# Optimization experiments

Hardware: AMD Instinct MI355X
Metric: run time of the kernel (lower is better)

The kernel has to match this reference:

```python
import jax, jax.numpy as jnp
import numpy as np

N, D_IN, D_QK, D_V = 8192, 1024, 128, 128

def setup_inputs() -> dict:
    key = jax.random.key(0)
    k1, k2, k3, k4 = jax.random.split(key, 4)
    return {
        "x": jax.random.normal(k1, (N, D_IN), dtype=jnp.float32),
        "W_q": jax.random.normal(k2, (D_IN, D_QK), dtype=jnp.float32),
        "W_k": jax.random.normal(k3, (D_IN, D_QK), dtype=jnp.float32),
        "W_v": jax.random.normal(k4, (D_IN, D_V), dtype=jnp.float32),
    }

def reference(x, W_q, W_k, W_v):
    Q = x @ W_q          # [N, d_qk]
    K = x @ W_k          # [N, d_qk]
    V = x @ W_v          # [N, d_v]
    scale = 1.0 / jnp.sqrt(jnp.asarray(W_q.shape[1], dtype=Q.dtype))
    S = jnp.einsum("nd,md->nm", Q, K) * scale  # [N, N]
    A = jax.nn.softmax(S, axis=1)
    return A @ V         # [N, d_v]
```

## Files before the change

kernel.cpp:

```cpp
#include <hip/hip_runtime.h>
#include <cstdint>
#include <cstddef>

#define NTOK 8192
#define DIN  1024
#define DH   128
#define KVB  64

typedef __attribute__((ext_vector_type(4))) float f32x4;
typedef __attribute__((ext_vector_type(16))) float f32x16;
typedef __bf16 bf16x8 __attribute__((ext_vector_type(8)));
typedef unsigned short u16x8 __attribute__((ext_vector_type(8)));
typedef unsigned int u32x4 __attribute__((ext_vector_type(4)));

__device__ __forceinline__ unsigned short f2bf(float f){
  union { float f; unsigned u; } x; x.f = f;
  unsigned r = x.u + 0x7FFFu + ((x.u >> 16) & 1u);
  return (unsigned short)(r >> 16);
}
__device__ __forceinline__ float bf2f(unsigned short b){
  union { unsigned u; float f; } x; x.u = ((unsigned)b) << 16;
  return x.f;
}
__device__ __forceinline__ unsigned cvtpk_bf16(float lo, float hi){
  unsigned r;
  asm volatile("v_cvt_pk_bf16_f32 %0, %1, %2" : "=v"(r) : "v"(lo), "v"(hi));
  return r;
}
__device__ __forceinline__ void gload16(const void* g, void* l){
  using gp_t = const __attribute__((address_space(1))) char*;
  using lp_t = __attribute__((address_space(3))) char*;
  __builtin_amdgcn_global_load_lds((gp_t)(uintptr_t)g, (lp_t)(uint32_t)(uintptr_t)l, 16, 0, 0);
}

__global__ void k_wsplit(const float* __restrict__ Wq, const float* __restrict__ Wk,
                         const float* __restrict__ Wv,
                         unsigned short* __restrict__ WhT, unsigned short* __restrict__ WlT){
  int e = blockIdx.x * 256 + threadIdx.x;
  int n = e >> 10, k = e & 1023;
  const float* W = (n < 128) ? Wq : ((n < 256) ? Wk : Wv);
  float v = W[(size_t)k * 128 + (n & 127)];
  unsigned short h = f2bf(v);
  WhT[e] = h;
  WlT[e] = f2bf(v - bf2f(h));
}

__global__ void k_xsplit(const float* __restrict__ x,
                         unsigned short* __restrict__ xh, unsigned short* __restrict__ xl){
  size_t i = ((size_t)blockIdx.x * 256 + threadIdx.x) * 8;
  f32x4 a = *(const f32x4*)(x + i);
  f32x4 b = *(const f32x4*)(x + i + 4);
  u16x8 h, l;
  #pragma unroll
  for (int j = 0; j < 4; ++j){
    unsigned short h0 = f2bf(a[j]); h[j] = h0;   l[j]   = f2bf(a[j] - bf2f(h0));
    unsigned short h1 = f2bf(b[j]); h[4+j] = h1; l[4+j] = f2bf(b[j] - bf2f(h1));
  }
  *(u16x8*)(xh + i) = h;
  *(u16x8*)(xl + i) = l;
}

__global__ __launch_bounds__(256, 3) void k_proj(
    const unsigned short* __restrict__ xh, const unsigned short* __restrict__ xl,
    const unsigned short* __restrict__ WhT, const unsigned short* __restrict__ WlT,
    unsigned short* __restrict__ Qh, unsigned short* __restrict__ Ql,
    unsigned short* __restrict__ Kh, unsigned short* __restrict__ Kl,
    unsigned short* __restrict__ Vt){
  __shared__ __align__(16) char smem[32768];
  const int lane = threadIdx.x & 63, wid = threadIdx.x >> 6;
  const int l15 = lane & 15, lk = lane >> 4;
  const int bm = blockIdx.x;
  const int by = blockIdx.y;
  const int bt = by >> 1, nh = by & 1;
  const int wm = wid >> 1, wn = wid & 1;

  const int srow = lane >> 3;
  const int gc8  = (lane & 7) ^ srow;
  const unsigned short* gsrc;
  char* ldst;
  int grow0;
  if (wid == 0){      gsrc = xh;  grow0 = bm*64;            ldst = smem; }
  else if (wid == 1){ gsrc = xl;  grow0 = bm*64;            ldst = smem + 8192; }
  else if (wid == 2){ gsrc = WhT; grow0 = bt*128 + nh*64;   ldst = smem + 16384; }
  else {              gsrc = WlT; grow0 = bt*128 + nh*64;   ldst = smem + 24576; }
  const unsigned short* gbase = gsrc + (size_t)(grow0 + srow)*DIN + gc8*8;
  const bool stage_on = (bt < 2) || (wid == 0) || (wid == 2);

  f32x4 acc[2][2] = {};

  for (int t = 0; t < 16; ++t){
    if (stage_on){
      #pragma unroll
      for (int i = 0; i < 8; ++i)
        gload16(gbase + (size_t)i*8*DIN + t*64, ldst + i*1024);
    }
    __syncthreads();

    bf16x8 a_h[2][2], a_l[2][2], b_h[2][2], b_l[2][2];
    const unsigned sw = (unsigned)(l15 & 7);
    #pragma unroll
    for (int mf = 0; mf < 2; ++mf)
      #pragma unroll
      for (int kc = 0; kc < 2; ++kc){
        unsigned rA = (unsigned)(wm*32 + mf*16 + l15);
        unsigned offA = rA*128u + ((((unsigned)(kc*4 + lk)) ^ sw)*16u);
        a_h[mf][kc] = *(const bf16x8*)(const void*)(smem + offA);
        unsigned rB = (unsigned)(wn*32 + mf*16 + l15);
        unsigned offB = rB*128u + ((((unsigned)(kc*4 + lk)) ^ sw)*16u);
        b_h[mf][kc] = *(const bf16x8*)(const void*)(smem + 16384 + offB);
        if (bt < 2){
          a_l[mf][kc] = *(const bf16x8*)(const void*)(smem + 8192 + offA);
          b_l[mf][kc] = *(const bf16x8*)(const void*)(smem + 24576 + offB);
        }
      }
    #pragma unroll
    for (int mf = 0; mf < 2; ++mf)
      #pragma unroll
      for (int nf = 0; nf < 2; ++nf)
        #pragma unroll
        for (int kc = 0; kc < 2; ++kc){
          acc[mf][nf] = __builtin_amdgcn_mfma_f32_16x16x32_bf16(a_h[mf][kc], b_h[nf][kc], acc[mf][nf], 0,0,0);
          if (bt < 2){
            acc[mf][nf] = __builtin_amdgcn_mfma_f32_16x16x32_bf16(a_h[mf][kc], b_l[nf][kc], acc[mf][nf], 0,0,0);
            acc[mf][nf] = __builtin_amdgcn_mfma_f32_16x16x32_bf16(a_l[mf][kc], b_h[nf][kc], acc[mf][nf], 0,0,0);
          }
        }
    __syncthreads();
  }

  const float qscale = 0.08838834764831845f;
  #pragma unroll
  for (int mf = 0; mf < 2; ++mf){
    #pragma unroll
    for (int nf = 0; nf < 2; ++nf){
      #pragma unroll
      for (int r = 0; r < 4; ++r){
        int row = bm*64 + wm*32 + mf*16 + lk*4 + r;
        int col = nh*64 + wn*32 + nf*16 + l15;
        float v = acc[mf][nf][r];
        if (bt == 0){
          v *= qscale;
          unsigned short h = f2bf(v);
          Qh[(size_t)row*DH + col] = h;
          Ql[(size_t)row*DH + col] = f2bf(v - bf2f(h));
        } else if (bt == 1){
          unsigned short h = f2bf(v);
          Kh[(size_t)row*DH + col] = h;
          Kl[(size_t)row*DH + col] = f2bf(v - bf2f(h));
        } else {
          Vt[(size_t)col*NTOK + row] = f2bf(v);
        }
      }
    }
  }
}

__global__ __launch_bounds__(256, 2) void k_flash(
    const unsigned short* __restrict__ Qh, const unsigned short* __restrict__ Ql,
    const unsigned short* __restrict__ Kh, const unsigned short* __restrict__ Kl,
    const unsigned short* __restrict__ Vt,
    float* __restrict__ Opart, float* __restrict__ mpart, float* __restrict__ lpart,
    int ksplit){
  __shared__ __align__(16) char smem[49152];
  char* smemc = smem;
  const int tid = threadIdx.x;
  const int lane = tid & 63, wid = tid >> 6;
  const int l31 = lane & 31, hi = lane >> 5;
  const int qb = blockIdx.x / ksplit, ks = blockIdx.x - qb*ksplit;
  const int q0w = qb*128 + wid*32;
  const int kvlen = NTOK / ksplit;
  const int kvbase = ks * kvlen;
  const int NT = kvlen / KVB;

  bf16x8 qh[8], ql[8];
  #pragma unroll
  for (int kc = 0; kc < 8; ++kc){
    size_t off = (size_t)(q0w + l31)*DH + kc*16 + hi*8;
    qh[kc] = *(const bf16x8*)(const void*)(Qh + off);
    ql[kc] = *(const bf16x8*)(const void*)(Ql + off);
  }

  int gK[4], gV[4], ldsO[4];
  #pragma unroll
  for (int i = 0; i < 4; ++i){
    int g = 4*wid + i;
    int rk = 4*g + (lane >> 4);
    gK[i] = rk*DH + (((lane & 15) ^ (rk & 7))*8);
    int rv = 8*g + (lane >> 3);
    gV[i] = rv*NTOK + (((lane & 7) ^ (lane >> 3))*8);
    ldsO[i] = g*1024;
  }

  #define STAGE(kv0_) do { int _o = (kv0_)*DH;                          \
    _Pragma("unroll")                                                   \
    for (int i = 0; i < 4; ++i){                                        \
      gload16(Kh + (size_t)(_o + gK[i]), smemc + ldsO[i]);              \
      gload16(Kl + (size_t)(_o + gK[i]), smemc + 16384 + ldsO[i]);      \
      gload16(Vt + (size_t)(gV[i] + (kv0_)), smemc + 32768 + ldsO[i]);  \
    } } while(0)

  STAGE(kvbase);
  __syncthreads();

  f32x16 o[4] = {};
  float m_run = -3.0e38f, l_run = 0.f;

  for (int t = 0; t < NT; ++t){
    f32x16 s0 = {}, s1 = {};
    __builtin_amdgcn_s_setprio(1);
    #pragma unroll
    for (int kc = 0; kc < 8; ++kc){
      int r0 = l31;
      unsigned off0 = (unsigned)r0*256u + ((((unsigned)(kc*2 + hi)) ^ (unsigned)(r0 & 7))*16u);
      bf16x8 kh0 = *(const bf16x8*)(const void*)(smemc + off0);
      bf16x8 kl0 = *(const bf16x8*)(const void*)(smemc + 16384 + off0);
      s0 = __builtin_amdgcn_mfma_f32_32x32x16_bf16(kh0, qh[kc], s0, 0,0,0);
      s0 = __builtin_amdgcn_mfma_f32_32x32x16_bf16(kl0, qh[kc], s0, 0,0,0);
      s0 = __builtin_amdgcn_mfma_f32_32x32x16_bf16(kh0, ql[kc], s0, 0,0,0);
      int r1 = 32 + l31;
      unsigned off1 = (unsigned)r1*256u + ((((unsigned)(kc*2 + hi)) ^ (unsigned)(r1 & 7))*16u);
      bf16x8 kh1 = *(const bf16x8*)(const void*)(smemc + off1);
      bf16x8 kl1 = *(const bf16x8*)(const void*)(smemc + 16384 + off1);
      s1 = __builtin_amdgcn_mfma_f32_32x32x16_bf16(kh1, qh[kc], s1, 0,0,0);
      s1 = __builtin_amdgcn_mfma_f32_32x32x16_bf16(kl1, qh[kc], s1, 0,0,0);
      s1 = __builtin_amdgcn_mfma_f32_32x32x16_bf16(kh1, ql[kc], s1, 0,0,0);
    }
    __builtin_amdgcn_s_setprio(0);

    float pmax = s0[0];
    #pragma unroll
    for (int i = 1; i < 16; ++i) pmax = fmaxf(pmax, s0[i]);
    #pragma unroll
    for (int i = 0; i < 16; ++i) pmax = fmaxf(pmax, s1[i]);
    pmax = fmaxf(pmax, __shfl_xor(pmax, 32));
    if (!__all(pmax - m_run <= 8.f)){
      float mnew = fmaxf(m_run, pmax);
      float corr = __expf(m_run - mnew);
      l_run *= corr;
      #pragma unroll
      for (int dblk = 0; dblk < 4; ++dblk)
        #pragma unroll
        for (int i = 0; i < 16; ++i) o[dblk][i] *= corr;
      m_run = mnew;
    }
    float tsum = 0.f;
    #pragma unroll
    for (int i = 0; i < 16; ++i){ s0[i] = __expf(s0[i] - m_run); tsum += s0[i]; }
    #pragma unroll
    for (int i = 0; i < 16; ++i){ s1[i] = __expf(s1[i] - m_run); tsum += s1[i]; }
    tsum += __shfl_xor(tsum, 32);
    l_run += tsum;

    __builtin_amdgcn_s_setprio(1);
    #pragma unroll
    for (int b = 0; b < 4; ++b){
      f32x16 sv = (b & 2) ? s1 : s0;
      const int base = 8*(b & 1);
      unsigned w0 = cvtpk_bf16(sv[base+0], sv[base+1]);
      unsigned w1 = cvtpk_bf16(sv[base+2], sv[base+3]);
      unsigned w2 = cvtpk_bf16(sv[base+4], sv[base+5]);
      unsigned w3 = cvtpk_bf16(sv[base+6], sv[base+7]);
      unsigned sx0 = (unsigned)__shfl_xor((int)w0, 32);
      unsigned sx1 = (unsigned)__shfl_xor((int)w1, 32);
      unsigned sx2 = (unsigned)__shfl_xor((int)w2, 32);
      unsigned sx3 = (unsigned)__shfl_xor((int)w3, 32);
      u32x4 pw;
      pw[0] = hi ? sx2 : w0;
      pw[1] = hi ? sx3 : w1;
      pw[2] = hi ? w2 : sx0;
      pw[3] = hi ? w3 : sx1;
      bf16x8 pB = __builtin_bit_cast(bf16x8, pw);
      #pragma unroll
      for (int dblk = 0; dblk < 4; ++dblk){
        int rv = dblk*32 + l31;
        unsigned offv = 32768u + (unsigned)rv*128u +
                        ((((unsigned)(b*2 + hi)) ^ (unsigned)(rv & 7))*16u);
        bf16x8 vf = *(const bf16x8*)(const void*)(smemc + offv);
        o[dblk] = __builtin_amdgcn_mfma_f32_32x32x16_bf16(vf, pB, o[dblk], 0,0,0);
      }
    }
    __builtin_amdgcn_s_setprio(0);

    __syncthreads();
    if (t + 1 < NT) STAGE(kvbase + (t+1)*KVB);
    __syncthreads();
  }
  #undef STAGE

  float* Op = Opart + ((size_t)ks*NTOK + q0w + l31)*DH;
  #pragma unroll
  for (int dblk = 0; dblk < 4; ++dblk)
    #pragma unroll
    for (int g = 0; g < 4; ++g){
      f32x4 q4 = { o[dblk][4*g+0], o[dblk][4*g+1], o[dblk][4*g+2], o[dblk][4*g+3] };
      *(f32x4*)(Op + dblk*32 + 8*g + 4*hi) = q4;
    }
  if (hi == 0){
    mpart[(size_t)ks*NTOK + q0w + l31] = m_run;
    lpart[(size_t)ks*NTOK + q0w + l31] = l_run;
  }
}

__global__ void k_merge(const float* __restrict__ Opart, const float* __restrict__ mpart,
                        const float* __restrict__ lpart, float* __restrict__ out, int ksplit){
  int gid = blockIdx.x*256 + threadIdx.x;
  int n = gid >> 5, c4 = (gid & 31) * 4;
  float M = -1e30f;
  for (int ks = 0; ks < ksplit; ++ks) M = fmaxf(M, mpart[(size_t)ks*NTOK + n]);
  float L = 0.f;
  f32x4 acc = {0.f, 0.f, 0.f, 0.f};
  for (int ks = 0; ks < ksplit; ++ks){
    float w = __expf(mpart[(size_t)ks*NTOK + n] - M);
    L += lpart[(size_t)ks*NTOK + n] * w;
    f32x4 op = *(const f32x4*)(Opart + ((size_t)ks*NTOK + n)*DH + c4);
    acc += op * w;
  }
  float inv = 1.f / L;
  *(f32x4*)(out + (size_t)n*DH + c4) = acc * inv;
}

extern "C" void kernel_launch(void* const* d_in, const int* in_sizes, int n_in,
                              void* d_out, int out_size, void* d_ws, size_t ws_size,
                              hipStream_t stream){
  const float* x  = (const float*)d_in[0];
  const float* Wq = (const float*)d_in[1];
  const float* Wk = (const float*)d_in[2];
  const float* Wv = (const float*)d_in[3];
  float* out = (float*)d_out;

  char* ws = (char*)d_ws;
  const size_t SZ_WT = (size_t)384*1024*2;
  const size_t SZ_X  = (size_t)NTOK*DIN*2;
  const size_t SZ_QK = (size_t)NTOK*DH*2;
  size_t off = 0;
  unsigned short* WhT = (unsigned short*)(ws + off); off += SZ_WT;
  unsigned short* WlT = (unsigned short*)(ws + off); off += SZ_WT;
  unsigned short* xh  = (unsigned short*)(ws + off); off += SZ_X;
  unsigned short* xl  = (unsigned short*)(ws + off); off += SZ_X;
  unsigned short* Qh  = (unsigned short*)(ws + off); off += SZ_QK;
  unsigned short* Ql  = (unsigned short*)(ws + off); off += SZ_QK;
  unsigned short* Kh  = (unsigned short*)(ws + off); off += SZ_QK;
  unsigned short* Kl  = (unsigned short*)(ws + off); off += SZ_QK;
  unsigned short* Vt  = (unsigned short*)(ws + off); off += SZ_QK;

  int ksplit = 8;
  while (ksplit > 1 &&
         off + (size_t)ksplit*(NTOK*(size_t)DH*4 + 2*NTOK*4) > ws_size)
    ksplit >>= 1;
  float* Opart = (float*)(ws + off); off += (size_t)ksplit*NTOK*DH*4;
  float* mpart = (float*)(ws + off); off += (size_t)ksplit*NTOK*4;
  float* lpart = (float*)(ws + off); off += (size_t)ksplit*NTOK*4;

  k_wsplit<<<dim3((384*1024)/256), dim3(256), 0, stream>>>(Wq, Wk, Wv, WhT, WlT);
  k_xsplit<<<dim3((NTOK*DIN)/(256*8)), dim3(256), 0, stream>>>(x, xh, xl);
  k_proj  <<<dim3(NTOK/64, 6), dim3(256), 0, stream>>>(xh, xl, WhT, WlT, Qh, Ql, Kh, Kl, Vt);
  k_flash <<<dim3((NTOK/128)*ksplit), dim3(256), 0, stream>>>(Qh, Ql, Kh, Kl, Vt,
                                                              Opart, mpart, lpart, ksplit);
  k_merge <<<dim3(NTOK*32/256), dim3(256), 0, stream>>>(Opart, mpart, lpart, out, ksplit);
}
```

Baseline: 184.0 us.

## Double-buffer K/V tiles in LDS and widen flash blocks to 512 threads

The flash kernel now uses 8 waves per block covering 256 query rows, so each K/V tile staged in LDS is shared by twice as many waves. LDS is doubled to hold two buffers, and the next tile's async load is issued before computing on the current one, which removes one barrier per iteration and overlaps global loads with MFMA work. The cost is 96KB of LDS per block and half as many blocks in the grid, which limits occupancy to one block per CU and may leave CUs idle.

```diff
diff --git a/kernel.cpp b/kernel.cpp
--- a/kernel.cpp
+++ b/kernel.cpp
@@ -155,19 +155,19 @@
   }
 }
 
-__global__ __launch_bounds__(256, 2) void k_flash(
+__global__ __launch_bounds__(512, 2) void k_flash(
     const unsigned short* __restrict__ Qh, const unsigned short* __restrict__ Ql,
     const unsigned short* __restrict__ Kh, const unsigned short* __restrict__ Kl,
     const unsigned short* __restrict__ Vt,
     float* __restrict__ Opart, float* __restrict__ mpart, float* __restrict__ lpart,
     int ksplit){
-  __shared__ __align__(16) char smem[49152];
+  __shared__ __align__(16) char smem[98304];
   char* smemc = smem;
   const int tid = threadIdx.x;
   const int lane = tid & 63, wid = tid >> 6;
   const int l31 = lane & 31, hi = lane >> 5;
   const int qb = blockIdx.x / ksplit, ks = blockIdx.x - qb*ksplit;
-  const int q0w = qb*128 + wid*32;
+  const int q0w = qb*256 + wid*32;
   const int kvlen = NTOK / ksplit;
   const int kvbase = ks * kvlen;
   const int NT = kvlen / KVB;
@@ -180,45 +180,50 @@
     ql[kc] = *(const bf16x8*)(const void*)(Ql + off);
   }
 
-  int gK[4], gV[4], ldsO[4];
-  #pragma unroll
-  for (int i = 0; i < 4; ++i){
-    int g = 4*wid + i;
-    int rk = 4*g + (lane >> 4);
-    gK[i] = rk*DH + (((lane & 15) ^ (rk & 7))*8);
-    int rv = 8*g + (lane >> 3);
-    gV[i] = rv*NTOK + (((lane & 7) ^ (lane >> 3))*8);
-    ldsO[i] = g*1024;
-  }
-
-  #define STAGE(kv0_) do { int _o = (kv0_)*DH;                          \
-    _Pragma("unroll")                                                   \
-    for (int i = 0; i < 4; ++i){                                        \
-      gload16(Kh + (size_t)(_o + gK[i]), smemc + ldsO[i]);              \
-      gload16(Kl + (size_t)(_o + gK[i]), smemc + 16384 + ldsO[i]);      \
-      gload16(Vt + (size_t)(gV[i] + (kv0_)), smemc + 32768 + ldsO[i]);  \
+  #define STAGE(kv0_, bufo_) do {                                          \
+    _Pragma("unroll")                                                      \
+    for (int i_ = 0; i_ < 6; ++i_){                                        \
+      int g_ = 6*wid + i_;                                                 \
+      const unsigned short* gp_; unsigned lo_;                             \
+      if (g_ < 16){                                                        \
+        int rk_ = 4*g_ + (lane >> 4);                                      \
+        gp_ = Kh + (size_t)(kv0_)*DH + rk_*DH + (((lane&15)^(rk_&7))*8);   \
+        lo_ = (unsigned)g_*1024u;                                          \
+      } else if (g_ < 32){                                                 \
+        int g2_ = g_ - 16; int rk_ = 4*g2_ + (lane >> 4);                  \
+        gp_ = Kl + (size_t)(kv0_)*DH + rk_*DH + (((lane&15)^(rk_&7))*8);   \
+        lo_ = 16384u + (unsigned)g2_*1024u;                                \
+      } else {                                                             \
+        int g2_ = g_ - 32; int rv_ = 8*g2_ + (lane >> 3);                  \
+        gp_ = Vt + (size_t)rv_*NTOK + (kv0_) + (((lane&7)^(lane>>3))*8);   \
+        lo_ = 32768u + (unsigned)g2_*1024u;                                \
+      }                                                                    \
+      gload16(gp_, smemc + (bufo_) + lo_);                                 \
     } } while(0)
 
-  STAGE(kvbase);
+  STAGE(kvbase, 0u);
   __syncthreads();
 
   f32x16 o[4] = {};
   float m_run = -3.0e38f, l_run = 0.f;
+  unsigned bufo = 0;
 
   for (int t = 0; t < NT; ++t){
+    if (t + 1 < NT) STAGE(kvbase + (t+1)*KVB, bufo ^ 49152u);
+
     f32x16 s0 = {}, s1 = {};
     __builtin_amdgcn_s_setprio(1);
     #pragma unroll
     for (int kc = 0; kc < 8; ++kc){
       int r0 = l31;
-      unsigned off0 = (unsigned)r0*256u + ((((unsigned)(kc*2 + hi)) ^ (unsigned)(r0 & 7))*16u);
+      unsigned off0 = bufo + (unsigned)r0*256u + ((((unsigned)(kc*2 + hi)) ^ (unsigned)(r0 & 7))*16u);
       bf16x8 kh0 = *(const bf16x8*)(const void*)(smemc + off0);
       bf16x8 kl0 = *(const bf16x8*)(const void*)(smemc + 16384 + off0);
       s0 = __builtin_amdgcn_mfma_f32_32x32x16_bf16(kh0, qh[kc], s0, 0,0,0);
       s0 = __builtin_amdgcn_mfma_f32_32x32x16_bf16(kl0, qh[kc], s0, 0,0,0);
       s0 = __builtin_amdgcn_mfma_f32_32x32x16_bf16(kh0, ql[kc], s0, 0,0,0);
       int r1 = 32 + l31;
-      unsigned off1 = (unsigned)r1*256u + ((((unsigned)(kc*2 + hi)) ^ (unsigned)(r1 & 7))*16u);
+      unsigned off1 = bufo + (unsigned)r1*256u + ((((unsigned)(kc*2 + hi)) ^ (unsigned)(r1 & 7))*16u);
       bf16x8 kh1 = *(const bf16x8*)(const void*)(smemc + off1);
       bf16x8 kl1 = *(const bf16x8*)(const void*)(smemc + 16384 + off1);
       s1 = __builtin_amdgcn_mfma_f32_32x32x16_bf16(kh1, qh[kc], s1, 0,0,0);
@@ -273,7 +278,7 @@
       #pragma unroll
       for (int dblk = 0; dblk < 4; ++dblk){
         int rv = dblk*32 + l31;
-        unsigned offv = 32768u + (unsigned)rv*128u +
+        unsigned offv = bufo + 32768u + (unsigned)rv*128u +
                         ((((unsigned)(b*2 + hi)) ^ (unsigned)(rv & 7))*16u);
         bf16x8 vf = *(const bf16x8*)(const void*)(smemc + offv);
         o[dblk] = __builtin_amdgcn_mfma_f32_32x32x16_bf16(vf, pB, o[dblk], 0,0,0);
@@ -282,8 +287,7 @@
     __builtin_amdgcn_s_setprio(0);
 
     __syncthreads();
-    if (t + 1 < NT) STAGE(kvbase + (t+1)*KVB);
-    __syncthreads();
+    bufo ^= 49152u;
   }
   #undef STAGE
 
@@ -354,7 +358,7 @@
   k_wsplit<<<dim3((384*1024)/256), dim3(256), 0, stream>>>(Wq, Wk, Wv, WhT, WlT);
   k_xsplit<<<dim3((NTOK*DIN)/(256*8)), dim3(256), 0, stream>>>(x, xh, xl);
   k_proj  <<<dim3(NTOK/64, 6), dim3(256), 0, stream>>>(xh, xl, WhT, WlT, Qh, Ql, Kh, Kl, Vt);
-  k_flash <<<dim3((NTOK/128)*ksplit), dim3(256), 0, stream>>>(Qh, Ql, Kh, Kl, Vt,
+  k_flash <<<dim3((NTOK/256)*ksplit), dim3(512), 0, stream>>>(Qh, Ql, Kh, Kl, Vt,
                                                               Opart, mpart, lpart, ksplit);
   k_merge <<<dim3(NTOK*32/256), dim3(256), 0, stream>>>(Opart, mpart, lpart, out, ksplit);
 }
```

Result: slower. 188.4 us (+2.4%).
